# Performance work log

Hardware: AMD Instinct MI355X
Metric: run time of the kernel (lower is better)

## Reference

```python
import jax, jax.numpy as jnp
import numpy as np

B, H, W, C = 16, 32, 32, 512
HEADS, DHEAD = 8, 64  # head * channel == C
GROUPS, EPS = 32, 1e-5


def setup_inputs() -> dict:
    key = jax.random.key(0)
    ks = jax.random.split(key, 6)
    return {
        "x": jax.random.normal(ks[0], (B, H, W, C), jnp.float32),
        "gn_gamma": jnp.ones((C,), jnp.float32),
        "gn_beta": jnp.zeros((C,), jnp.float32),
        "wq": jax.random.normal(ks[1], (C, HEADS * DHEAD), jnp.float32) * 0.02,
        "wk": jax.random.normal(ks[2], (C, HEADS * DHEAD), jnp.float32) * 0.02,
        "wv": jax.random.normal(ks[3], (C, HEADS * DHEAD), jnp.float32) * 0.02,
        "conv_w": jax.random.normal(ks[4], (3, 3, HEADS * DHEAD, C), jnp.float32) * 0.02,
        "conv_b": jnp.zeros((C,), jnp.float32),
    }


def _group_norm(x, gamma, beta):
    b, h, w, c = x.shape
    xg = x.reshape(b, h, w, GROUPS, c // GROUPS)
    mean = jnp.mean(xg, axis=(1, 2, 4), keepdims=True)
    var = jnp.var(xg, axis=(1, 2, 4), keepdims=True)
    xn = (xg - mean) * jax.lax.rsqrt(var + EPS)
    return xn.reshape(b, h, w, c) * gamma + beta


def reference(x, gn_gamma, gn_beta, wq, wk, wv, conv_w, conv_b):
    xn = _group_norm(x, gn_gamma, gn_beta)          # [B,H,W,C]
    t = xn.reshape(B, H * W, C)                      # tokens [B,S,C]
    q = (t @ wq).reshape(B, H * W, HEADS, DHEAD)
    k = (t @ wk).reshape(B, H * W, HEADS, DHEAD)
    v = (t @ wv).reshape(B, H * W, HEADS, DHEAD)
    scale = 1.0 / jnp.sqrt(jnp.asarray(DHEAD, q.dtype))
    scores = jnp.einsum("bqhd,bkhd->bhqk", q, k) * scale  # [B,HEADS,S,S]
    weights = jax.nn.softmax(scores, axis=-1)
    out = jnp.einsum("bhqk,bkhd->bqhd", weights, v)       # [B,S,HEADS,DHEAD]
    out = out.reshape(B, H, W, HEADS * DHEAD)
    y = jax.lax.conv_general_dilated(
        out, conv_w, window_strides=(1, 1), padding=((1, 1), (1, 1)),
        dimension_numbers=("NHWC", "HWIO", "NHWC")) + conv_b
    return y + x
```

## Files before the change

### kernel.cpp

```cpp
#include <hip/hip_runtime.h>
#include <hip/hip_bf16.h>

#define Bn 16
#define Cc 512
#define Ss 1024
#define HEADS 8
#define DHEAD 64
#define GROUPS 32
#define CPG 16
#define EPSv 1e-5f
#define Mtok (Bn*Ss)
#define QKVS 1536
#define PROW 34
#define PIMG (PROW*PROW)

typedef __hip_bfloat16 bf16;
typedef __attribute__((ext_vector_type(8))) short short8;
typedef __attribute__((ext_vector_type(4))) float f32x4;

union U4 { uint4 u; bf16 h[8]; };
union B4 { ushort4 u; bf16 h[4]; };

__device__ __forceinline__ void stage16(const bf16* g, bf16* l) {
    __builtin_amdgcn_global_load_lds((const __attribute__((address_space(1))) void*)g,
                                     (__attribute__((address_space(3))) void*)l,
                                     16, 0, 0);
}

__device__ __forceinline__ unsigned int pkbf(float a, float b) {
    union { __hip_bfloat16 h; unsigned short u; } ua, ub;
    ua.h = __float2bfloat16(a); ub.h = __float2bfloat16(b);
    return ((unsigned int)ub.u << 16) | ua.u;
}

__global__ __launch_bounds__(256) void wtrans(const float* __restrict__ src,
                                              bf16* __restrict__ dst) {
    size_t off = (size_t)blockIdx.y * 262144;
    int t = blockIdx.x * 256 + threadIdx.x;
    int n = t & 511, k8 = (t >> 9) * 8;
    const float* s = src + off + (size_t)k8 * 512 + n;
    U4 o;
#pragma unroll
    for (int j = 0; j < 8; j++) o.h[j] = __float2bfloat16(s[(size_t)j * 512]);
    *(uint4*)(dst + off + (size_t)n * 512 + k8) = o.u;
}

__global__ __launch_bounds__(256) void gn_stats(const float* __restrict__ x,
                                                float* __restrict__ stats) {
    int bg = blockIdx.x;
    int b = bg >> 5, g = bg & 31;
    int tid = threadIdx.x;
    const size_t base = (size_t)b * Ss * Cc + g * CPG;
    float sum = 0.f, sq = 0.f;
    for (int i = tid; i < 4096; i += 256) {
        int s = i >> 2, c4 = (i & 3) * 4;
        float4 t = *(const float4*)(x + base + (size_t)s * Cc + c4);
        sum += t.x + t.y + t.z + t.w;
        sq  += t.x * t.x + t.y * t.y + t.z * t.z + t.w * t.w;
    }
    __shared__ float s1[4], s2[4];
#pragma unroll
    for (int off = 32; off > 0; off >>= 1) {
        sum += __shfl_down(sum, off);
        sq  += __shfl_down(sq,  off);
    }
    if ((tid & 63) == 0) { s1[tid >> 6] = sum; s2[tid >> 6] = sq; }
    __syncthreads();
    if (tid == 0) {
        float S = s1[0] + s1[1] + s1[2] + s1[3];
        float Q = s2[0] + s2[1] + s2[2] + s2[3];
        float mean = S * (1.f / 16384.f);
        float var  = Q * (1.f / 16384.f) - mean * mean;
        stats[bg * 2 + 0] = mean;
        stats[bg * 2 + 1] = rsqrtf(var + EPSv);
    }
}

__global__ __launch_bounds__(256) void gn_apply(const float* __restrict__ x,
                                                const float* __restrict__ stats,
                                                const float* __restrict__ gamma,
                                                const float* __restrict__ beta,
                                                bf16* __restrict__ xn) {
    size_t i = (size_t)blockIdx.x * 256 + threadIdx.x;
    size_t e = i * 4;
    int c0 = (int)(e & (Cc - 1));
    int token = (int)(e >> 9);
    int b = token >> 10;
    int g = c0 >> 4;
    float mean = stats[(b * 32 + g) * 2 + 0];
    float rstd = stats[(b * 32 + g) * 2 + 1];
    float4 t  = *(const float4*)(x + e);
    float4 gm = *(const float4*)(gamma + c0);
    float4 bt = *(const float4*)(beta + c0);
    B4 o;
    o.h[0] = __float2bfloat16((t.x - mean) * rstd * gm.x + bt.x);
    o.h[1] = __float2bfloat16((t.y - mean) * rstd * gm.y + bt.y);
    o.h[2] = __float2bfloat16((t.z - mean) * rstd * gm.z + bt.z);
    o.h[3] = __float2bfloat16((t.w - mean) * rstd * gm.w + bt.w);
    *(ushort4*)(xn + e) = o.u;
}

__global__ __launch_bounds__(256) void zero_pad(bf16* __restrict__ Pad) {
    int idx = blockIdx.x * 256 + threadIdx.x;
    int b = idx / (132 * 64);
    int rem = idx - b * 132 * 64;
    int t = rem >> 6, seg = rem & 63;
    int r, c;
    if (t < 34)      { r = 0;  c = t; }
    else if (t < 68) { r = 33; c = t - 34; }
    else { int u = t - 68; r = 1 + (u >> 1); c = (u & 1) * 33; }
    uint4 z = {0u, 0u, 0u, 0u};
    *(uint4*)(Pad + ((size_t)b * PIMG + r * PROW + c) * Cc + seg * 8) = z;
}

__global__ __launch_bounds__(256) void gemm_qkv(const bf16* __restrict__ A,
                                                const bf16* __restrict__ Wt,
                                                bf16* __restrict__ C) {
    __shared__ __align__(16) bf16 As[128][32];
    __shared__ __align__(16) bf16 Bs[128][32];
    int tid = threadIdx.x;
    int wave = tid >> 6, lane = tid & 63;
    int l15 = lane & 15, quad = lane >> 4;
    int wm = wave >> 1, wn = wave & 1;
    int m0 = blockIdx.y * 128, n0 = blockIdx.x * 128;
    int lr = lane >> 2, kseg = (lane & 3) * 8;
    int ar0 = wave * 32 + lr;

    const bf16* ga = A  + (size_t)(m0 + ar0) * Cc + kseg;
    const bf16* gb = Wt + (size_t)(n0 + ar0) * Cc + kseg;
    bf16* la0 = &As[wave * 32][0];
    bf16* la1 = &As[wave * 32 + 16][0];
    bf16* lb0 = &Bs[wave * 32][0];
    bf16* lb1 = &Bs[wave * 32 + 16][0];

    f32x4 acc[4][4] = {};
    for (int k0 = 0; k0 < 512; k0 += 32) {
        __syncthreads();
        stage16(ga + k0,                  la0);
        stage16(ga + k0 + (size_t)16 * Cc, la1);
        stage16(gb + k0,                  lb0);
        stage16(gb + k0 + (size_t)16 * Cc, lb1);
        __syncthreads();
        short8 af[4], bfv[4];
#pragma unroll
        for (int mt = 0; mt < 4; mt++) af[mt]  = *(const short8*)&As[wm * 64 + mt * 16 + l15][quad * 8];
#pragma unroll
        for (int nt = 0; nt < 4; nt++) bfv[nt] = *(const short8*)&Bs[wn * 64 + nt * 16 + l15][quad * 8];
#pragma unroll
        for (int mt = 0; mt < 4; mt++)
#pragma unroll
            for (int nt = 0; nt < 4; nt++)
                acc[mt][nt] = __builtin_amdgcn_mfma_f32_16x16x32_bf16(af[mt], bfv[nt], acc[mt][nt], 0, 0, 0);
    }
#pragma unroll
    for (int mt = 0; mt < 4; mt++)
#pragma unroll
        for (int r = 0; r < 4; r++) {
            size_t row = (size_t)(m0 + wm * 64 + mt * 16 + quad * 4 + r) * QKVS + n0 + wn * 64 + l15;
#pragma unroll
            for (int nt = 0; nt < 4; nt++)
                C[row + nt * 16] = __float2bfloat16(acc[mt][nt][r]);
        }
}

__global__ __launch_bounds__(256) void attention_mfma(const bf16* __restrict__ QKV,
                                                      bf16* __restrict__ Pad) {
    int blk = blockIdx.x;
    int qt = blk & 15;
    int bh = blk >> 4;
    int h = bh & (HEADS - 1), b = bh >> 3;
    int tid = threadIdx.x;
    int wave = tid >> 6, lane = tid & 63;
    int l15 = lane & 15, quad = lane >> 4;

    __shared__ __align__(16) bf16 Ks[2][32][72];
    __shared__ __align__(16) bf16 Vt[2][64][40];

    const size_t base = (size_t)b * Ss * QKVS + h * DHEAD;
    const bf16* kbase = QKV + base + 512;
    const bf16* vbase = QKV + base + 1024;

    int q0 = qt * 64 + wave * 16;
    const bf16* qrow = QKV + base + (size_t)(q0 + l15) * QKVS + quad * 8;
    short8 qf0 = *(const short8*)(qrow);
    short8 qf1 = *(const short8*)(qrow + 32);

    f32x4 oaccT[4] = {{0.f,0.f,0.f,0.f},{0.f,0.f,0.f,0.f},{0.f,0.f,0.f,0.f},{0.f,0.f,0.f,0.f}};
    float lsum = 0.f;
    const f32x4 zero4 = {0.f, 0.f, 0.f, 0.f};

    int tok = tid & 31, d0 = (tid >> 5) * 8;

    int srcA = (((quad * 2) & 3) * 16 + l15);
    int srcB = (((quad * 2 + 1) & 3) * 16 + l15);

    uint4 nk, nv;
    {
        const size_t rb = (size_t)tok * QKVS + d0;
        nk = *(const uint4*)(kbase + rb);
        nv = *(const uint4*)(vbase + rb);
    }
    *(uint4*)&Ks[0][tok][d0] = nk;
    { U4 u; u.u = nv;
#pragma unroll
      for (int i = 0; i < 8; i++) Vt[0][d0 + i][tok] = u.h[i]; }
    __syncthreads();

    for (int c = 0; c < 32; ++c) {
        int buf = c & 1;
        if (c + 1 < 32) {
            const size_t rb = (size_t)((c + 1) * 32 + tok) * QKVS + d0;
            nk = *(const uint4*)(kbase + rb);
            nv = *(const uint4*)(vbase + rb);
        }
        unsigned int pk[2][2];
#pragma unroll
        for (int kb = 0; kb < 2; kb++) {
            short8 kf0 = *(const short8*)&Ks[buf][kb * 16 + l15][quad * 8];
            short8 kf1 = *(const short8*)&Ks[buf][kb * 16 + l15][32 + quad * 8];
            f32x4 s = __builtin_amdgcn_mfma_f32_16x16x32_bf16(kf0, qf0, zero4, 0, 0, 0);
            s = __builtin_amdgcn_mfma_f32_16x16x32_bf16(kf1, qf1, s, 0, 0, 0);
            float p0 = __expf(s[0] * 0.125f);
            float p1 = __expf(s[1] * 0.125f);
            float p2 = __expf(s[2] * 0.125f);
            float p3 = __expf(s[3] * 0.125f);
            lsum += (p0 + p1) + (p2 + p3);
            pk[kb][0] = pkbf(p0, p1);
            pk[kb][1] = pkbf(p2, p3);
        }
        unsigned int a0 = __shfl((int)pk[0][0], srcA);
        unsigned int a1 = __shfl((int)pk[0][1], srcA);
        unsigned int a2 = __shfl((int)pk[1][0], srcA);
        unsigned int a3 = __shfl((int)pk[1][1], srcA);
        unsigned int b0 = __shfl((int)pk[0][0], srcB);
        unsigned int b1 = __shfl((int)pk[0][1], srcB);
        unsigned int b2 = __shfl((int)pk[1][0], srcB);
        unsigned int b3 = __shfl((int)pk[1][1], srcB);
        union { short8 s8; unsigned int u[4]; } PT;
        bool lo = (quad < 2);
        PT.u[0] = lo ? a0 : a2;
        PT.u[1] = lo ? a1 : a3;
        PT.u[2] = lo ? b0 : b2;
        PT.u[3] = lo ? b1 : b3;
#pragma unroll
        for (int dt = 0; dt < 4; dt++) {
            short8 vf = *(const short8*)&Vt[buf][dt * 16 + l15][quad * 8];
            oaccT[dt] = __builtin_amdgcn_mfma_f32_16x16x32_bf16(vf, PT.s8, oaccT[dt], 0, 0, 0);
        }
        if (c + 1 < 32) {
            *(uint4*)&Ks[buf ^ 1][tok][d0] = nk;
            U4 u; u.u = nv;
#pragma unroll
            for (int i = 0; i < 8; i++) Vt[buf ^ 1][d0 + i][tok] = u.h[i];
        }
        __syncthreads();
    }

    lsum += __shfl_xor(lsum, 16);
    lsum += __shfl_xor(lsum, 32);
    float inv = 1.f / lsum;

    int s = q0 + l15;
    size_t rowoff = ((size_t)(b * PROW + (s >> 5) + 1) * PROW + (s & 31) + 1) * Cc + h * DHEAD;
#pragma unroll
    for (int dt = 0; dt < 4; dt++) {
        B4 o;
#pragma unroll
        for (int r = 0; r < 4; r++) o.h[r] = __float2bfloat16(oaccT[dt][r] * inv);
        *(ushort4*)(Pad + rowoff + dt * 16 + quad * 4) = o.u;
    }
}

__global__ __launch_bounds__(256, 2) void conv_mfma(const bf16* __restrict__ Pad,
                                                    const bf16* __restrict__ Wct,
                                                    const float* __restrict__ bias,
                                                    const float* __restrict__ xres,
                                                    float* __restrict__ out) {
    __shared__ __align__(16) bf16 As[2][136 * 32];
    __shared__ __align__(16) bf16 Bs[2][3][128][32];

    int tid = threadIdx.x;
    int wave = tid >> 6, lane = tid & 63;
    int l15 = lane & 15, quad = lane >> 4;
    int wm = wave >> 1, wn = wave & 1;
    int m0 = blockIdx.y * 128, n0 = blockIdx.x * 128;
    int b = m0 >> 10, oh0 = (m0 & 1023) >> 5;

    int lr = lane >> 2, kseg = (lane & 3) * 8;
    const bf16* gwp = Wct + (size_t)(n0 + wave * 32 + lr) * Cc + kseg;

    int t1 = tid >> 2,          r1 = t1 / 34, col1 = t1 - r1 * 34;
    int t2 = (tid + 256) >> 2,  r2 = t2 / 34, col2 = t2 - r2 * 34;
    int t3 = (tid + 512) >> 2,  r3 = t3 / 34, col3 = t3 - r3 * 34;
    int ks = (tid & 3) * 8;
    const size_t dyStride = (size_t)PROW * Cc;
    const bf16* pA1 = Pad + ((size_t)b * PIMG + (size_t)(oh0 + r1) * PROW + col1) * Cc + ks;
    const bf16* pA2 = Pad + ((size_t)b * PIMG + (size_t)(oh0 + r2) * PROW + col2) * Cc + ks;
    const bf16* pA3 = Pad + ((size_t)b * PIMG + (size_t)(oh0 + r3) * PROW + col3) * Cc + ks;

    int arow[4];
#pragma unroll
    for (int mt = 0; mt < 4; mt++)
        arow[mt] = (wm * 2 + (mt >> 1)) * 34 + (mt & 1) * 16 + l15;

    auto stage_it = [&](int it, int p) {
        int dyi = it >> 4;
        int k0 = (it & 15) << 5;
        size_t aoff = (size_t)dyi * dyStride + k0;
        stage16(pA1 + aoff, &As[p][wave * 512]);
        stage16(pA2 + aoff, &As[p][2048 + wave * 512]);
        if (tid < 32) stage16(pA3 + aoff, &As[p][4096]);
        const bf16* gW = gwp + (size_t)(dyi * 3) * (Cc * Cc) + k0;
#pragma unroll
        for (int t = 0; t < 3; t++) {
            const bf16* gwt = gW + (size_t)t * (Cc * Cc);
            stage16(gwt,                   &Bs[p][t][wave * 32][0]);
            stage16(gwt + (size_t)16 * Cc, &Bs[p][t][wave * 32 + 16][0]);
        }
    };

    f32x4 acc[4][4] = {};
    stage_it(0, 0);
    for (int it = 0; it < 48; ++it) {
        int p = it & 1;
        if (it + 1 < 48) {
            stage_it(it + 1, p ^ 1);
            asm volatile("s_waitcnt vmcnt(8)" ::: "memory");
        } else {
            asm volatile("s_waitcnt vmcnt(0)" ::: "memory");
        }
        __builtin_amdgcn_s_barrier();

        short8 af[3][4], bfv[3][4];
#pragma unroll
        for (int dxi = 0; dxi < 3; dxi++) {
#pragma unroll
            for (int mt = 0; mt < 4; mt++)
                af[dxi][mt] = *(const short8*)&As[p][(arow[mt] + dxi) * 32 + quad * 8];
#pragma unroll
            for (int nt = 0; nt < 4; nt++)
                bfv[dxi][nt] = *(const short8*)&Bs[p][dxi][wn * 64 + nt * 16 + l15][quad * 8];
        }
        asm volatile("s_waitcnt lgkmcnt(0)" ::: "memory");
        __builtin_amdgcn_sched_barrier(0);
        __builtin_amdgcn_s_barrier();

#pragma unroll
        for (int dxi = 0; dxi < 3; dxi++)
#pragma unroll
            for (int mt = 0; mt < 4; mt++)
#pragma unroll
                for (int nt = 0; nt < 4; nt++)
                    acc[mt][nt] = __builtin_amdgcn_mfma_f32_16x16x32_bf16(af[dxi][mt], bfv[dxi][nt], acc[mt][nt], 0, 0, 0);
    }

#pragma unroll
    for (int mt = 0; mt < 4; mt++)
#pragma unroll
        for (int r = 0; r < 4; r++) {
            size_t row = (size_t)(m0 + wm * 64 + mt * 16 + quad * 4 + r) * Cc + n0 + wn * 64 + l15;
#pragma unroll
            for (int nt = 0; nt < 4; nt++) {
                int n = n0 + wn * 64 + nt * 16 + l15;
                out[row + nt * 16] = acc[mt][nt][r] + bias[n] + xres[row + nt * 16];
            }
        }
}

extern "C" void kernel_launch(void* const* d_in, const int* in_sizes, int n_in,
                              void* d_out, int out_size, void* d_ws, size_t ws_size,
                              hipStream_t stream) {
    const float* x     = (const float*)d_in[0];
    const float* gamma = (const float*)d_in[1];
    const float* beta  = (const float*)d_in[2];
    const float* wq    = (const float*)d_in[3];
    const float* wk    = (const float*)d_in[4];
    const float* wv    = (const float*)d_in[5];
    const float* convw = (const float*)d_in[6];
    const float* convb = (const float*)d_in[7];
    float* out = (float*)d_out;

    char* ws = (char*)d_ws;
    bf16*  pad   = (bf16*)ws;
    float* stats = (float*)ws;
    bf16*  xn    = (bf16*)(ws + 4096);
    bf16*  wt    = (bf16*)(ws + 4096 + ((size_t)16 << 20));
    bf16*  qkv   = (bf16*)(ws + ((size_t)19 << 20));
    bf16*  wct   = (bf16*)(ws + ((size_t)67 << 20));

    wtrans<<<dim3(128, 1), 256, 0, stream>>>(wq, wt);
    wtrans<<<dim3(128, 1), 256, 0, stream>>>(wk, wt + 262144);
    wtrans<<<dim3(128, 1), 256, 0, stream>>>(wv, wt + 524288);
    wtrans<<<dim3(128, 9), 256, 0, stream>>>(convw, wct);

    gn_stats<<<dim3(Bn * GROUPS), 256, 0, stream>>>(x, stats);
    gn_apply<<<dim3(Mtok * Cc / (4 * 256)), 256, 0, stream>>>(x, stats, gamma, beta, xn);

    gemm_qkv<<<dim3(QKVS / 128, Mtok / 128), 256, 0, stream>>>(xn, wt, qkv);

    zero_pad<<<dim3(528), 256, 0, stream>>>(pad);
    attention_mfma<<<dim3(Bn * HEADS * (Ss / 64)), 256, 0, stream>>>(qkv, pad);

    conv_mfma<<<dim3(Cc / 128, Mtok / 128), 256, 0, stream>>>(pad, wct, convb, x, out);
}
```

Baseline: 326.2 us.

## Write V transposed from QKV GEMM and async-stage K/V tiles in attention

The QKV GEMM epilogue now writes Q and K into a 1024-wide buffer and V into a separate head-major transposed buffer. Attention can then stage both K and V into LDS directly with global_load_lds, using an XOR swizzle and double buffering, instead of going through registers and doing a scalar LDS transpose of V. The KV tile grows from 32 to 64 keys per iteration, with explicit vmcnt waits, s_barrier and setprio hints. This removes the per-element V transpose and the register round trip, in exchange for strided transposed stores in the GEMM epilogue and more complex synchronisation.

```diff
diff --git a/kernel.cpp b/kernel.cpp
--- a/kernel.cpp
+++ b/kernel.cpp
@@ -11,6 +11,7 @@
 #define EPSv 1e-5f
 #define Mtok (Bn*Ss)
 #define QKVS 1536
+#define QKS 1024
 #define PROW 34
 #define PIMG (PROW*PROW)
 
@@ -115,7 +116,8 @@
 
 __global__ __launch_bounds__(256) void gemm_qkv(const bf16* __restrict__ A,
                                                 const bf16* __restrict__ Wt,
-                                                bf16* __restrict__ C) {
+                                                bf16* __restrict__ C,
+                                                bf16* __restrict__ vT) {
     __shared__ __align__(16) bf16 As[128][32];
     __shared__ __align__(16) bf16 Bs[128][32];
     int tid = threadIdx.x;
@@ -152,18 +154,38 @@
             for (int nt = 0; nt < 4; nt++)
                 acc[mt][nt] = __builtin_amdgcn_mfma_f32_16x16x32_bf16(af[mt], bfv[nt], acc[mt][nt], 0, 0, 0);
     }
-#pragma unroll
-    for (int mt = 0; mt < 4; mt++)
-#pragma unroll
-        for (int r = 0; r < 4; r++) {
-            size_t row = (size_t)(m0 + wm * 64 + mt * 16 + quad * 4 + r) * QKVS + n0 + wn * 64 + l15;
-#pragma unroll
-            for (int nt = 0; nt < 4; nt++)
-                C[row + nt * 16] = __float2bfloat16(acc[mt][nt][r]);
-        }
-}
-
-__global__ __launch_bounds__(256) void attention_mfma(const bf16* __restrict__ QKV,
+
+    if (n0 < 1024) {
+#pragma unroll
+        for (int mt = 0; mt < 4; mt++)
+#pragma unroll
+            for (int r = 0; r < 4; r++) {
+                size_t row = (size_t)(m0 + wm * 64 + mt * 16 + quad * 4 + r) * QKS + n0 + wn * 64 + l15;
+#pragma unroll
+                for (int nt = 0; nt < 4; nt++)
+                    C[row + nt * 16] = __float2bfloat16(acc[mt][nt][r]);
+            }
+    } else {
+        int hh = ((n0 - 1024) >> 6) + wn;
+        int bq = m0 >> 10;
+        int tok0 = (m0 & 1023) + wm * 64;
+#pragma unroll
+        for (int nt = 0; nt < 4; nt++) {
+            int d = nt * 16 + l15;
+            bf16* drow = vT + (size_t)(hh * 64 + d) * 16384 + bq * 1024 + tok0;
+#pragma unroll
+            for (int mt = 0; mt < 4; mt++) {
+                B4 o;
+#pragma unroll
+                for (int r = 0; r < 4; r++) o.h[r] = __float2bfloat16(acc[mt][nt][r]);
+                *(ushort4*)(drow + mt * 16 + quad * 4) = o.u;
+            }
+        }
+    }
+}
+
+__global__ __launch_bounds__(256) void attention_mfma(const bf16* __restrict__ QK,
+                                                      const bf16* __restrict__ vT,
                                                       bf16* __restrict__ Pad) {
     int blk = blockIdx.x;
     int qt = blk & 15;
@@ -173,51 +195,58 @@
     int wave = tid >> 6, lane = tid & 63;
     int l15 = lane & 15, quad = lane >> 4;
 
-    __shared__ __align__(16) bf16 Ks[2][32][72];
-    __shared__ __align__(16) bf16 Vt[2][64][40];
-
-    const size_t base = (size_t)b * Ss * QKVS + h * DHEAD;
-    const bf16* kbase = QKV + base + 512;
-    const bf16* vbase = QKV + base + 1024;
+    __shared__ __align__(16) bf16 KT[2][4096];
+    __shared__ __align__(16) bf16 VTs[2][4096];
+
+    const size_t base = (size_t)b * Ss * QKS + h * DHEAD;
+    const bf16* kbase = QK + base + 512;
 
     int q0 = qt * 64 + wave * 16;
-    const bf16* qrow = QKV + base + (size_t)(q0 + l15) * QKVS + quad * 8;
+    const bf16* qrow = QK + base + (size_t)(q0 + l15) * QKS + quad * 8;
     short8 qf0 = *(const short8*)(qrow);
     short8 qf1 = *(const short8*)(qrow + 32);
+
+    int r1 = tid >> 3,         f1 = (tid & 7) ^ (r1 & 7);
+    int r2 = (tid + 256) >> 3, f2 = ((tid + 256) & 7) ^ (r2 & 7);
+    const bf16* gk1 = kbase + (size_t)r1 * QKS + f1 * 8;
+    const bf16* gk2 = kbase + (size_t)r2 * QKS + f2 * 8;
+    const bf16* gv1 = vT + (size_t)(h * 64 + r1) * 16384 + b * 1024 + f1 * 8;
+    const bf16* gv2 = vT + (size_t)(h * 64 + r2) * 16384 + b * 1024 + f2 * 8;
 
     f32x4 oaccT[4] = {{0.f,0.f,0.f,0.f},{0.f,0.f,0.f,0.f},{0.f,0.f,0.f,0.f},{0.f,0.f,0.f,0.f}};
     float lsum = 0.f;
     const f32x4 zero4 = {0.f, 0.f, 0.f, 0.f};
-
-    int tok = tid & 31, d0 = (tid >> 5) * 8;
-
-    int srcA = (((quad * 2) & 3) * 16 + l15);
-    int srcB = (((quad * 2 + 1) & 3) * 16 + l15);
-
-    uint4 nk, nv;
-    {
-        const size_t rb = (size_t)tok * QKVS + d0;
-        nk = *(const uint4*)(kbase + rb);
-        nv = *(const uint4*)(vbase + rb);
-    }
-    *(uint4*)&Ks[0][tok][d0] = nk;
-    { U4 u; u.u = nv;
-#pragma unroll
-      for (int i = 0; i < 8; i++) Vt[0][d0 + i][tok] = u.h[i]; }
-    __syncthreads();
-
-    for (int c = 0; c < 32; ++c) {
-        int buf = c & 1;
-        if (c + 1 < 32) {
-            const size_t rb = (size_t)((c + 1) * 32 + tok) * QKVS + d0;
-            nk = *(const uint4*)(kbase + rb);
-            nv = *(const uint4*)(vbase + rb);
-        }
-        unsigned int pk[2][2];
-#pragma unroll
-        for (int kb = 0; kb < 2; kb++) {
-            short8 kf0 = *(const short8*)&Ks[buf][kb * 16 + l15][quad * 8];
-            short8 kf1 = *(const short8*)&Ks[buf][kb * 16 + l15][32 + quad * 8];
+    int srcA = ((quad & 1) * 2) * 16 + l15;
+    int srcB = srcA + 16;
+    bool hiq = (quad >= 2);
+    int sw = l15 & 7;
+
+    auto stage = [&](int c0, int p) {
+        stage16(gk1 + (size_t)c0 * QKS, &KT[p][wave * 512]);
+        stage16(gk2 + (size_t)c0 * QKS, &KT[p][2048 + wave * 512]);
+        stage16(gv1 + c0,               &VTs[p][wave * 512]);
+        stage16(gv2 + c0,               &VTs[p][2048 + wave * 512]);
+    };
+
+    stage(0, 0);
+    for (int it = 0; it < 16; ++it) {
+        int p = it & 1;
+        if (it + 1 < 16) {
+            stage((it + 1) * 64, p ^ 1);
+            asm volatile("s_waitcnt vmcnt(4)" ::: "memory");
+        } else {
+            asm volatile("s_waitcnt vmcnt(0)" ::: "memory");
+        }
+        __builtin_amdgcn_s_barrier();
+        __builtin_amdgcn_sched_barrier(0);
+
+        unsigned int pk[4][2];
+        __builtin_amdgcn_s_setprio(1);
+#pragma unroll
+        for (int kb = 0; kb < 4; kb++) {
+            const bf16* kr = &KT[p][(kb * 16 + l15) * 64];
+            short8 kf0 = *(const short8*)(kr + ((quad ^ sw) * 8));
+            short8 kf1 = *(const short8*)(kr + (((4 + quad) ^ sw) * 8));
             f32x4 s = __builtin_amdgcn_mfma_f32_16x16x32_bf16(kf0, qf0, zero4, 0, 0, 0);
             s = __builtin_amdgcn_mfma_f32_16x16x32_bf16(kf1, qf1, s, 0, 0, 0);
             float p0 = __expf(s[0] * 0.125f);
@@ -228,32 +257,38 @@
             pk[kb][0] = pkbf(p0, p1);
             pk[kb][1] = pkbf(p2, p3);
         }
-        unsigned int a0 = __shfl((int)pk[0][0], srcA);
-        unsigned int a1 = __shfl((int)pk[0][1], srcA);
-        unsigned int a2 = __shfl((int)pk[1][0], srcA);
-        unsigned int a3 = __shfl((int)pk[1][1], srcA);
-        unsigned int b0 = __shfl((int)pk[0][0], srcB);
-        unsigned int b1 = __shfl((int)pk[0][1], srcB);
-        unsigned int b2 = __shfl((int)pk[1][0], srcB);
-        unsigned int b3 = __shfl((int)pk[1][1], srcB);
-        union { short8 s8; unsigned int u[4]; } PT;
-        bool lo = (quad < 2);
-        PT.u[0] = lo ? a0 : a2;
-        PT.u[1] = lo ? a1 : a3;
-        PT.u[2] = lo ? b0 : b2;
-        PT.u[3] = lo ? b1 : b3;
+        __builtin_amdgcn_s_setprio(0);
+
+        union { short8 s8; unsigned int u[4]; } PT0, PT1;
+        {
+            unsigned int A0 = __shfl((int)pk[0][0], srcA), A1 = __shfl((int)pk[0][1], srcA);
+            unsigned int A2 = __shfl((int)pk[1][0], srcA), A3 = __shfl((int)pk[1][1], srcA);
+            unsigned int B0 = __shfl((int)pk[0][0], srcB), B1 = __shfl((int)pk[0][1], srcB);
+            unsigned int B2 = __shfl((int)pk[1][0], srcB), B3 = __shfl((int)pk[1][1], srcB);
+            PT0.u[0] = hiq ? A2 : A0;  PT0.u[1] = hiq ? A3 : A1;
+            PT0.u[2] = hiq ? B2 : B0;  PT0.u[3] = hiq ? B3 : B1;
+            unsigned int C0 = __shfl((int)pk[2][0], srcA), C1 = __shfl((int)pk[2][1], srcA);
+            unsigned int C2 = __shfl((int)pk[3][0], srcA), C3 = __shfl((int)pk[3][1], srcA);
+            unsigned int D0 = __shfl((int)pk[2][0], srcB), D1 = __shfl((int)pk[2][1], srcB);
+            unsigned int D2 = __shfl((int)pk[3][0], srcB), D3 = __shfl((int)pk[3][1], srcB);
+            PT1.u[0] = hiq ? C2 : C0;  PT1.u[1] = hiq ? C3 : C1;
+            PT1.u[2] = hiq ? D2 : D0;  PT1.u[3] = hiq ? D3 : D1;
+        }
+
+        __builtin_amdgcn_s_setprio(1);
 #pragma unroll
         for (int dt = 0; dt < 4; dt++) {
-            short8 vf = *(const short8*)&Vt[buf][dt * 16 + l15][quad * 8];
-            oaccT[dt] = __builtin_amdgcn_mfma_f32_16x16x32_bf16(vf, PT.s8, oaccT[dt], 0, 0, 0);
-        }
-        if (c + 1 < 32) {
-            *(uint4*)&Ks[buf ^ 1][tok][d0] = nk;
-            U4 u; u.u = nv;
-#pragma unroll
-            for (int i = 0; i < 8; i++) Vt[buf ^ 1][d0 + i][tok] = u.h[i];
-        }
-        __syncthreads();
+            const bf16* vr = &VTs[p][(dt * 16 + l15) * 64];
+            short8 vf0 = *(const short8*)(vr + ((quad ^ sw) * 8));
+            short8 vf1 = *(const short8*)(vr + (((4 + quad) ^ sw) * 8));
+            oaccT[dt] = __builtin_amdgcn_mfma_f32_16x16x32_bf16(vf0, PT0.s8, oaccT[dt], 0, 0, 0);
+            oaccT[dt] = __builtin_amdgcn_mfma_f32_16x16x32_bf16(vf1, PT1.s8, oaccT[dt], 0, 0, 0);
+        }
+        __builtin_amdgcn_s_setprio(0);
+
+        __builtin_amdgcn_sched_barrier(0);
+        __builtin_amdgcn_s_barrier();
+        __builtin_amdgcn_sched_barrier(0);
     }
 
     lsum += __shfl_xor(lsum, 16);
@@ -385,7 +420,8 @@
     float* stats = (float*)ws;
     bf16*  xn    = (bf16*)(ws + 4096);
     bf16*  wt    = (bf16*)(ws + 4096 + ((size_t)16 << 20));
-    bf16*  qkv   = (bf16*)(ws + ((size_t)19 << 20));
+    bf16*  qk    = (bf16*)(ws + ((size_t)19 << 20));
+    bf16*  vt    = (bf16*)(ws + ((size_t)51 << 20));
     bf16*  wct   = (bf16*)(ws + ((size_t)67 << 20));
 
     wtrans<<<dim3(128, 1), 256, 0, stream>>>(wq, wt);
@@ -396,10 +432,10 @@
     gn_stats<<<dim3(Bn * GROUPS), 256, 0, stream>>>(x, stats);
     gn_apply<<<dim3(Mtok * Cc / (4 * 256)), 256, 0, stream>>>(x, stats, gamma, beta, xn);
 
-    gemm_qkv<<<dim3(QKVS / 128, Mtok / 128), 256, 0, stream>>>(xn, wt, qkv);
+    gemm_qkv<<<dim3(QKVS / 128, Mtok / 128), 256, 0, stream>>>(xn, wt, qk, vt);
 
     zero_pad<<<dim3(528), 256, 0, stream>>>(pad);
-    attention_mfma<<<dim3(Bn * HEADS * (Ss / 64)), 256, 0, stream>>>(qkv, pad);
+    attention_mfma<<<dim3(Bn * HEADS * (Ss / 64)), 256, 0, stream>>>(qk, vt, pad);
 
     conv_mfma<<<dim3(Cc / 128, Mtok / 128), 256, 0, stream>>>(pad, wct, convb, x, out);
 }
```

New measurement: 312.8 us. -4.1%, faster.
